# Kernel optimization log

Hardware: AMD Instinct MI355X
Metric: run time of the kernel (lower is better)

## Reference

```python
import jax, jax.numpy as jnp
import numpy as np

B, LQ, LK, DK, DV = 32, 128, 4096, 256, 256


def setup_inputs() -> dict:
    key = jax.random.key(0)
    k1, k2, k3, k4, k5 = jax.random.split(key, 5)
    return {
        "query": jax.random.normal(k1, (B, LQ, DK), dtype=jnp.float32),
        "query_lengths": jax.random.randint(k2, (B,), 1, LQ, dtype=jnp.int32),
        "keys": jax.random.normal(k3, (B, LK, DK), dtype=jnp.float32),
        "values": jax.random.normal(k4, (B, LK, DV), dtype=jnp.float32),
        "mask": jax.random.randint(k5, (B, LK), 0, 2, dtype=jnp.int32),  # 1 = masked out
    }


def reference(query, query_lengths, keys, values, mask):
    # zero query positions beyond each example's length (torch: mask_query masked_fill 0)
    q_valid = jnp.arange(query.shape[1])[None, :] < query_lengths[:, None]  # [B, Lq]
    query = jnp.where(q_valid[:, :, None], query, 0.0)
    # zero masked key/value timesteps (torch mask: 1 -> masked)
    kv_valid = (mask == 0)[:, :, None]  # [B, Lk, 1]
    keys = jnp.where(kv_valid, keys, 0.0)
    values = jnp.where(kv_valid, values, 0.0)
    # attention scores [B, Lq, Lk]
    weights = jnp.einsum("bqd,bkd->bqk", query, keys)
    # exact-zero scores (masked rows/cols) -> -inf, matching torch weights==0.0 fill
    weights = jnp.where(weights == 0.0, -jnp.inf, weights)
    weights = jax.nn.softmax(weights, axis=-1)
    # rows that were all -inf produce NaN -> cleaned to 0
    weights = jnp.where(jnp.isnan(weights), 0.0, weights)
    attended = jnp.einsum("bqk,bkv->bqv", weights, values)  # [B, Lq, Dv]
    return jnp.mean(attended, axis=1)  # [B, Dv]
```

## Files before the change

kernel.cpp:

```cpp
#include <hip/hip_runtime.h>
#include <hip/hip_fp16.h>
#include <stdint.h>

#define NB  32
#define NLQ 128
#define NLK 4096
#define NDK 256
#define NDV 256
#define KT  32
#define SPLITS 8
#define MINSPLITS 4

typedef _Float16 f16;
typedef _Float16 f16x4 __attribute__((ext_vector_type(4)));
typedef _Float16 f16x8 __attribute__((ext_vector_type(8)));
typedef float    f32x4 __attribute__((ext_vector_type(4)));

__global__ __launch_bounds__(512) void fvta_part1(
    const float* __restrict__ q_, const float* __restrict__ k_,
    const float* __restrict__ v_, const int* __restrict__ mask_,
    f16* __restrict__ accw, float* __restrict__ mlw)
{
    __shared__ __align__(16) f16 KA[2][KT * NDK];
    __shared__ __align__(16) f16 VA[2][KT * NDV];
    __shared__ int MK[NLK / MINSPLITS];

    const int tid = threadIdx.x, w = tid >> 6, lane = tid & 63;
    const int l15 = lane & 15, lhi = lane >> 4;
    const int qsub = w >> 1;
    const int dvh  = w & 1;
    const int x = blockIdx.x, b = blockIdx.y;
    const int S = gridDim.x >> 1;
    const int s = x >> 1, qz = x & 1;
    const int slice = NLK / S, nt = slice / KT, kbase = s * slice;
    const float NEG = -__builtin_inff();

    const float* kb = k_ + ((size_t)b * NLK + kbase) * NDK;
    const float* vb = v_ + ((size_t)b * NLK + kbase) * NDV;
    const int*   mb = mask_ + b * NLK + kbase;

    for (int i = tid; i < slice; i += 512) MK[i] = mb[i];

    f16x8 qf[8];
    {
        const float* qrow = q_ + ((size_t)b * NLQ + qz * 64 + qsub * 16 + l15) * NDK
                          + lhi * 8;
        #pragma unroll
        for (int kd = 0; kd < 8; ++kd) {
            f32x4 xv = *(const f32x4*)(qrow + kd * 32);
            f32x4 yv = *(const f32x4*)(qrow + kd * 32 + 4);
            f16x8 f;
            f[0]=(f16)xv[0]; f[1]=(f16)xv[1]; f[2]=(f16)xv[2]; f[3]=(f16)xv[3];
            f[4]=(f16)yv[0]; f[5]=(f16)yv[1]; f[6]=(f16)yv[2]; f[7]=(f16)yv[3];
            qf[kd] = f;
        }
    }

    f32x4 accu[8];
    #pragma unroll
    for (int i = 0; i < 8; ++i) accu[i] = (f32x4){0.f, 0.f, 0.f, 0.f};
    float m_run = NEG, l_run = 0.f;

    f32x4 ks[4], vs[4];

    auto stage = [&](f16* KAb, f16* VAb) {
        #pragma unroll
        for (int r = 0; r < 4; ++r) {
            const int idx = r * 512 + tid;
            const int kk  = idx >> 6;
            const int d   = (idx & 63) * 4;
            const int e   = kk * NDK + (d ^ ((kk & 15) << 3));
            f32x4 xv = ks[r];
            f16x4 hh; hh[0]=(f16)xv[0]; hh[1]=(f16)xv[1]; hh[2]=(f16)xv[2]; hh[3]=(f16)xv[3];
            *(f16x4*)(KAb + e) = hh;
            f32x4 yv = vs[r];
            f16x4 gg; gg[0]=(f16)yv[0]; gg[1]=(f16)yv[1]; gg[2]=(f16)yv[2]; gg[3]=(f16)yv[3];
            *(f16x4*)(VAb + e) = gg;
        }
    };

    #pragma unroll
    for (int r = 0; r < 4; ++r) {
        ks[r] = *(const f32x4*)(kb + (r * 512 + tid) * 4);
        vs[r] = *(const f32x4*)(vb + (r * 512 + tid) * 4);
    }
    stage(KA[0], VA[0]);
    __syncthreads();

    const int swz = l15 << 3;

    for (int t = 0; t < nt; ++t) {
        const int cur = t & 1;
        if (t + 1 < nt) {
            const float* ksrc = kb + (size_t)(t + 1) * KT * NDK;
            const float* vsrc = vb + (size_t)(t + 1) * KT * NDV;
            #pragma unroll
            for (int r = 0; r < 4; ++r) {
                ks[r] = *(const f32x4*)(ksrc + (r * 512 + tid) * 4);
                vs[r] = *(const f32x4*)(vsrc + (r * 512 + tid) * 4);
            }
        }
        const int k0 = t * KT;

        f32x4 s4a = (f32x4){0.f,0.f,0.f,0.f}, s4b = s4a;
        {
            const f16* k0p = &KA[cur][(0 * 16 + l15) * NDK];
            const f16* k1p = &KA[cur][(1 * 16 + l15) * NDK];
            #pragma unroll
            for (int kd = 0; kd < 8; ++kd) {
                const int col = (kd * 32 + lhi * 8) ^ swz;
                f16x8 kfa = *(const f16x8*)(k0p + col);
                s4a = __builtin_amdgcn_mfma_f32_16x16x32_f16(kfa, qf[kd], s4a, 0, 0, 0);
                f16x8 kfb = *(const f16x8*)(k1p + col);
                s4b = __builtin_amdgcn_mfma_f32_16x16x32_f16(kfb, qf[kd], s4b, 0, 0, 0);
            }
        }

        const int4 m4a = *(const int4*)(MK + k0 + lhi * 4);
        const int4 m4b = *(const int4*)(MK + k0 + 16 + lhi * 4);
        float sa[4], sb[4];
        sa[0] = m4a.x ? NEG : s4a[0]; sa[1] = m4a.y ? NEG : s4a[1];
        sa[2] = m4a.z ? NEG : s4a[2]; sa[3] = m4a.w ? NEG : s4a[3];
        sb[0] = m4b.x ? NEG : s4b[0]; sb[1] = m4b.y ? NEG : s4b[1];
        sb[2] = m4b.z ? NEG : s4b[2]; sb[3] = m4b.w ? NEG : s4b[3];

        float tmax = fmaxf(fmaxf(fmaxf(sa[0], sa[1]), fmaxf(sa[2], sa[3])),
                           fmaxf(fmaxf(sb[0], sb[1]), fmaxf(sb[2], sb[3])));
        tmax = fmaxf(tmax, __shfl_xor(tmax, 16, 64));
        tmax = fmaxf(tmax, __shfl_xor(tmax, 32, 64));

        const bool defer = (m_run != NEG) && __all(tmax - m_run <= 8.f);
        if (!defer) {
            const float mnew = fmaxf(m_run, tmax);
            if (mnew != NEG) {
                const float scale = (m_run == NEG) ? 0.f : __expf(m_run - mnew);
                float scj[4];
                #pragma unroll
                for (int j = 0; j < 4; ++j) scj[j] = __shfl(scale, lhi * 4 + j, 64);
                #pragma unroll
                for (int d = 0; d < 8; ++d) {
                    accu[d][0] *= scj[0]; accu[d][1] *= scj[1];
                    accu[d][2] *= scj[2]; accu[d][3] *= scj[3];
                }
                l_run *= scale;
                m_run = mnew;
            }
        }

        float p4a[4], p4b[4];
        if (m_run == NEG) {
            #pragma unroll
            for (int j = 0; j < 4; ++j) { p4a[j] = 0.f; p4b[j] = 0.f; }
        } else {
            #pragma unroll
            for (int j = 0; j < 4; ++j) {
                p4a[j] = __expf(sa[j] - m_run);
                p4b[j] = __expf(sb[j] - m_run);
            }
        }
        float ps = (p4a[0] + p4a[1]) + (p4a[2] + p4a[3])
                 + (p4b[0] + p4b[1]) + (p4b[2] + p4b[3]);
        ps += __shfl_xor(ps, 16, 64);
        ps += __shfl_xor(ps, 32, 64);
        l_run += ps;

        f16x4 pa, pb;
        pa[0]=(f16)p4a[0]; pa[1]=(f16)p4a[1]; pa[2]=(f16)p4a[2]; pa[3]=(f16)p4a[3];
        pb[0]=(f16)p4b[0]; pb[1]=(f16)p4b[1]; pb[2]=(f16)p4b[2]; pb[3]=(f16)p4b[3];

        {
            const f16* VL = &VA[cur][0];
            #pragma unroll
            for (int h = 0; h < 2; ++h) {
                const f16x4 pfrag = h ? pb : pa;
                #pragma unroll
                for (int dg = 0; dg < 2; ++dg) {
                    #pragma unroll
                    for (int dd = 0; dd < 4; ++dd) {
                        f16x4 vf;
                        #pragma unroll
                        for (int j = 0; j < 4; ++j) {
                            const int rr  = lhi * 4 + j;
                            const int row = h * 16 + rr;
                            const int col = (dvh * 128 + (dg * 4 + dd) * 16 + l15)
                                            ^ (rr << 3);
                            vf[j] = VL[row * NDV + col];
                        }
                        accu[dg * 4 + dd] = __builtin_amdgcn_mfma_f32_16x16x16f16(
                            pfrag, vf, accu[dg * 4 + dd], 0, 0, 0);
                    }
                }
            }
        }

        if (t + 1 < nt) stage(KA[cur ^ 1], VA[cur ^ 1]);
        __syncthreads();
    }

    const float rl = (l_run > 0.f) ? 1.f / l_run : 0.f;
    float rlj[4];
    #pragma unroll
    for (int j = 0; j < 4; ++j) rlj[j] = __shfl(rl, lhi * 4 + j, 64);

    const size_t base = (size_t)(b * S + s) * NLQ + qz * 64 + qsub * 16;
    #pragma unroll
    for (int j = 0; j < 4; ++j) {
        f16* dst = accw + (base + lhi * 4 + j) * NDV + dvh * 128 + l15;
        #pragma unroll
        for (int d = 0; d < 8; ++d) dst[d * 16] = (f16)(accu[d][j] * rlj[j]);
    }
    if (dvh == 0 && lane < 16) {
        mlw[(base + lane) * 2]     = m_run;
        mlw[(base + lane) * 2 + 1] = l_run;
    }
}

__global__ __launch_bounds__(256) void fvta_merge(
    const f16* __restrict__ accw, const float* __restrict__ mlw,
    const int* __restrict__ qlen_, float* __restrict__ out_, int S)
{
    __shared__ float fac[8][SPLITS + 1];
    const int qc = blockIdx.x, b = blockIdx.y, tid = threadIdx.x;
    const int len = qlen_[b];
    const float NEG = -__builtin_inff();

    if (tid < 8) {
        const int q = qc * 8 + tid;
        if (q < len) {
            float gm = NEG;
            for (int ss = 0; ss < S; ++ss)
                gm = fmaxf(gm, mlw[((size_t)(b * S + ss) * NLQ + q) * 2]);
            float L = 0.f;
            for (int ss = 0; ss < S; ++ss) {
                const float m = mlw[((size_t)(b * S + ss) * NLQ + q) * 2];
                const float l = mlw[((size_t)(b * S + ss) * NLQ + q) * 2 + 1];
                if (m != NEG) L += l * __expf(m - gm);
            }
            for (int ss = 0; ss < S; ++ss) {
                const float m = mlw[((size_t)(b * S + ss) * NLQ + q) * 2];
                const float l = mlw[((size_t)(b * S + ss) * NLQ + q) * 2 + 1];
                fac[tid][ss] = (gm != NEG && L > 0.f && m != NEG)
                             ? l * __expf(m - gm) / L : 0.f;
            }
        } else {
            for (int ss = 0; ss < S; ++ss) fac[tid][ss] = 0.f;
        }
    }
    __syncthreads();

    float sum = 0.f;
    for (int qq = 0; qq < 8; ++qq) {
        const int q = qc * 8 + qq;
        for (int ss = 0; ss < S; ++ss) {
            const float f = fac[qq][ss];
            if (f != 0.f)
                sum += (float)accw[((size_t)(b * S + ss) * NLQ + q) * NDV + tid] * f;
        }
    }
    atomicAdd(&out_[b * NDV + tid], sum * (1.f / NLQ));
}

extern "C" void kernel_launch(void* const* d_in, const int* in_sizes, int n_in,
                              void* d_out, int out_size, void* d_ws, size_t ws_size,
                              hipStream_t stream) {
    const float* q    = (const float*)d_in[0];
    const int*   qlen = (const int*)d_in[1];
    const float* k    = (const float*)d_in[2];
    const float* v    = (const float*)d_in[3];
    const int*   mask = (const int*)d_in[4];
    float* out = (float*)d_out;

    int S = SPLITS;
    while (S > MINSPLITS &&
           ((size_t)NB * S * NLQ * NDV * 2 + (size_t)NB * S * NLQ * 8) > ws_size)
        S >>= 1;
    f16*   accw = (f16*)d_ws;
    float* mlw  = (float*)((char*)d_ws + (size_t)NB * S * NLQ * NDV * 2);

    hipMemsetAsync(out, 0, (size_t)out_size * sizeof(float), stream);
    dim3 g1(2 * S, NB);
    fvta_part1<<<g1, 512, 0, stream>>>(q, k, v, mask, accw, mlw);
    dim3 g2(NLQ / 8, NB);
    fvta_merge<<<g2, 256, 0, stream>>>(accw, mlw, qlen, out, S);
}
```

Measured before the change: 127.8 us.

## Store V transposed in LDS and use 16x16x32 MFMA for PV

V tiles are now loaded column-wise from global memory, each thread reading 16 strided floats, and written to LDS in a transposed, k-grouped layout. The PV product can then read contiguous f16x8 fragments and issue 8 MFMA 16x16x32 ops instead of 16 MFMA 16x16x16 ops fed by scalar LDS gathers. The P fragment is rebuilt with lane shuffles to match the new operand layout. The cost is uncoalesced strided global loads of V and extra shuffle work per tile.

```diff
diff --git a/kernel.cpp b/kernel.cpp
--- a/kernel.cpp
+++ b/kernel.cpp
@@ -12,6 +12,7 @@
 #define MINSPLITS 4
 
 typedef _Float16 f16;
+typedef _Float16 f16x2 __attribute__((ext_vector_type(2)));
 typedef _Float16 f16x4 __attribute__((ext_vector_type(4)));
 typedef _Float16 f16x8 __attribute__((ext_vector_type(8)));
 typedef float    f32x4 __attribute__((ext_vector_type(4)));
@@ -22,7 +23,7 @@
     f16* __restrict__ accw, float* __restrict__ mlw)
 {
     __shared__ __align__(16) f16 KA[2][KT * NDK];
-    __shared__ __align__(16) f16 VA[2][KT * NDV];
+    __shared__ __align__(16) f16 VT[2][4 * NDV * 8];
     __shared__ int MK[NLK / MINSPLITS];
 
     const int tid = threadIdx.x, w = tid >> 6, lane = tid & 63;
@@ -61,9 +62,11 @@
     for (int i = 0; i < 8; ++i) accu[i] = (f32x4){0.f, 0.f, 0.f, 0.f};
     float m_run = NEG, l_run = 0.f;
 
-    f32x4 ks[4], vs[4];
-
-    auto stage = [&](f16* KAb, f16* VAb) {
+    f32x4 ks[4];
+    float vsv[16];
+    const int dvv = tid >> 1, gv = tid & 1;
+
+    auto stageK = [&](f16* KAb) {
         #pragma unroll
         for (int r = 0; r < 4; ++r) {
             const int idx = r * 512 + tid;
@@ -73,33 +76,35 @@
             f32x4 xv = ks[r];
             f16x4 hh; hh[0]=(f16)xv[0]; hh[1]=(f16)xv[1]; hh[2]=(f16)xv[2]; hh[3]=(f16)xv[3];
             *(f16x4*)(KAb + e) = hh;
-            f32x4 yv = vs[r];
-            f16x4 gg; gg[0]=(f16)yv[0]; gg[1]=(f16)yv[1]; gg[2]=(f16)yv[2]; gg[3]=(f16)yv[3];
-            *(f16x4*)(VAb + e) = gg;
         }
     };
-
-    #pragma unroll
-    for (int r = 0; r < 4; ++r) {
-        ks[r] = *(const f32x4*)(kb + (r * 512 + tid) * 4);
-        vs[r] = *(const f32x4*)(vb + (r * 512 + tid) * 4);
-    }
-    stage(KA[0], VA[0]);
+    auto stageV = [&](f16* VTb) {
+        f16x8 lo, hi;
+        #pragma unroll
+        for (int i = 0; i < 8; ++i) { lo[i] = (f16)vsv[i]; hi[i] = (f16)vsv[8 + i]; }
+        *(f16x8*)(VTb + (2 * gv)     * (NDV * 8) + dvv * 8) = lo;
+        *(f16x8*)(VTb + (2 * gv + 1) * (NDV * 8) + dvv * 8) = hi;
+    };
+    auto loadKV = [&](int t) {
+        const float* ksrc = kb + (size_t)t * KT * NDK;
+        #pragma unroll
+        for (int r = 0; r < 4; ++r)
+            ks[r] = *(const f32x4*)(ksrc + (r * 512 + tid) * 4);
+        const float* vsrc = vb + (size_t)t * KT * NDV + gv * 16 * NDV + dvv;
+        #pragma unroll
+        for (int i = 0; i < 16; ++i)
+            vsv[i] = vsrc[i * NDV];
+    };
+
+    loadKV(0);
+    stageK(KA[0]); stageV(VT[0]);
     __syncthreads();
 
     const int swz = l15 << 3;
 
     for (int t = 0; t < nt; ++t) {
         const int cur = t & 1;
-        if (t + 1 < nt) {
-            const float* ksrc = kb + (size_t)(t + 1) * KT * NDK;
-            const float* vsrc = vb + (size_t)(t + 1) * KT * NDV;
-            #pragma unroll
-            for (int r = 0; r < 4; ++r) {
-                ks[r] = *(const f32x4*)(ksrc + (r * 512 + tid) * 4);
-                vs[r] = *(const f32x4*)(vsrc + (r * 512 + tid) * 4);
-            }
-        }
+        if (t + 1 < nt) loadKV(t + 1);
         const int k0 = t * KT;
 
         f32x4 s4a = (f32x4){0.f,0.f,0.f,0.f}, s4b = s4a;
@@ -164,36 +169,38 @@
         ps += __shfl_xor(ps, 32, 64);
         l_run += ps;
 
-        f16x4 pa, pb;
-        pa[0]=(f16)p4a[0]; pa[1]=(f16)p4a[1]; pa[2]=(f16)p4a[2]; pa[3]=(f16)p4a[3];
-        pb[0]=(f16)p4b[0]; pb[1]=(f16)p4b[1]; pb[2]=(f16)p4b[2]; pb[3]=(f16)p4b[3];
-
+        f16x8 pfrag;
         {
-            const f16* VL = &VA[cur][0];
-            #pragma unroll
-            for (int h = 0; h < 2; ++h) {
-                const f16x4 pfrag = h ? pb : pa;
-                #pragma unroll
-                for (int dg = 0; dg < 2; ++dg) {
-                    #pragma unroll
-                    for (int dd = 0; dd < 4; ++dd) {
-                        f16x4 vf;
-                        #pragma unroll
-                        for (int j = 0; j < 4; ++j) {
-                            const int rr  = lhi * 4 + j;
-                            const int row = h * 16 + rr;
-                            const int col = (dvh * 128 + (dg * 4 + dd) * 16 + l15)
-                                            ^ (rr << 3);
-                            vf[j] = VL[row * NDV + col];
-                        }
-                        accu[dg * 4 + dd] = __builtin_amdgcn_mfma_f32_16x16x16f16(
-                            pfrag, vf, accu[dg * 4 + dd], 0, 0, 0);
-                    }
-                }
-            }
-        }
-
-        if (t + 1 < nt) stage(KA[cur ^ 1], VA[cur ^ 1]);
+            union PU { f16x2 h; int u; } A0, A1, B0, B1;
+            A0.h[0]=(f16)p4a[0]; A0.h[1]=(f16)p4a[1];
+            A1.h[0]=(f16)p4a[2]; A1.h[1]=(f16)p4a[3];
+            B0.h[0]=(f16)p4b[0]; B0.h[1]=(f16)p4b[1];
+            B1.h[0]=(f16)p4b[2]; B1.h[1]=(f16)p4b[3];
+            const int sf = l15 + ((lhi & 1) << 5);
+            const int ss = sf + 16;
+            const int a0 = __shfl(A0.u, sf, 64), a1 = __shfl(A1.u, sf, 64);
+            const int b0 = __shfl(B0.u, sf, 64), b1 = __shfl(B1.u, sf, 64);
+            const int a2 = __shfl(A0.u, ss, 64), a3 = __shfl(A1.u, ss, 64);
+            const int b2 = __shfl(B0.u, ss, 64), b3 = __shfl(B1.u, ss, 64);
+            const bool useB = (lhi >= 2);
+            union PW { int u[4]; f16x8 v; } pw;
+            pw.u[0] = useB ? b0 : a0; pw.u[1] = useB ? b1 : a1;
+            pw.u[2] = useB ? b2 : a2; pw.u[3] = useB ? b3 : a3;
+            pfrag = pw.v;
+        }
+
+        {
+            const f16* vbase = &VT[cur][0] + lhi * (NDV * 8)
+                             + (dvh * 128 + l15) * 8;
+            #pragma unroll
+            for (int dc = 0; dc < 8; ++dc) {
+                f16x8 vf = *(const f16x8*)(vbase + dc * 16 * 8);
+                accu[dc] = __builtin_amdgcn_mfma_f32_16x16x32_f16(
+                    pfrag, vf, accu[dc], 0, 0, 0);
+            }
+        }
+
+        if (t + 1 < nt) { stageK(KA[cur ^ 1]); stageV(VT[cur ^ 1]); }
         __syncthreads();
     }
 
```

Result: slower. 138.3 us (+8.2%).

## Stage only half of V in LDS; read other half directly from global

Applied to the files above, without the earlier changes.

Only the first 128 value columns are staged into LDS as fp16. Waves handling the upper half load their V fragments straight from global memory inside the PV loop and convert them in registers. This halves the V shared-memory footprint and staging stores, which may improve occupancy. In exchange, the global loads sit on the critical path with uncoalesced strided access and no prefetch, so latency may be exposed.

```diff
diff --git a/kernel.cpp b/kernel.cpp
--- a/kernel.cpp
+++ b/kernel.cpp
@@ -22,7 +22,7 @@
     f16* __restrict__ accw, float* __restrict__ mlw)
 {
     __shared__ __align__(16) f16 KA[2][KT * NDK];
-    __shared__ __align__(16) f16 VA[2][KT * NDV];
+    __shared__ __align__(16) f16 VA[2][KT * 128];
     __shared__ int MK[NLK / MINSPLITS];
 
     const int tid = threadIdx.x, w = tid >> 6, lane = tid & 63;
@@ -61,7 +61,7 @@
     for (int i = 0; i < 8; ++i) accu[i] = (f32x4){0.f, 0.f, 0.f, 0.f};
     float m_run = NEG, l_run = 0.f;
 
-    f32x4 ks[4], vs[4];
+    f32x4 ks[4], vs[2];
 
     auto stage = [&](f16* KAb, f16* VAb) {
         #pragma unroll
@@ -73,17 +73,34 @@
             f32x4 xv = ks[r];
             f16x4 hh; hh[0]=(f16)xv[0]; hh[1]=(f16)xv[1]; hh[2]=(f16)xv[2]; hh[3]=(f16)xv[3];
             *(f16x4*)(KAb + e) = hh;
+        }
+        #pragma unroll
+        for (int r = 0; r < 2; ++r) {
+            const int idx = r * 512 + tid;
+            const int kk  = idx >> 5;
+            const int d   = (idx & 31) * 4;
+            const int e   = kk * 128 + (d ^ ((kk & 15) << 3));
             f32x4 yv = vs[r];
             f16x4 gg; gg[0]=(f16)yv[0]; gg[1]=(f16)yv[1]; gg[2]=(f16)yv[2]; gg[3]=(f16)yv[3];
             *(f16x4*)(VAb + e) = gg;
         }
     };
-
-    #pragma unroll
-    for (int r = 0; r < 4; ++r) {
-        ks[r] = *(const f32x4*)(kb + (r * 512 + tid) * 4);
-        vs[r] = *(const f32x4*)(vb + (r * 512 + tid) * 4);
-    }
+    auto loadKV = [&](int t) {
+        const float* ksrc = kb + (size_t)t * KT * NDK;
+        #pragma unroll
+        for (int r = 0; r < 4; ++r)
+            ks[r] = *(const f32x4*)(ksrc + (r * 512 + tid) * 4);
+        const float* vsrc = vb + (size_t)t * KT * NDV;
+        #pragma unroll
+        for (int r = 0; r < 2; ++r) {
+            const int idx = r * 512 + tid;
+            const int kk  = idx >> 5;
+            const int d   = (idx & 31) * 4;
+            vs[r] = *(const f32x4*)(vsrc + kk * NDV + d);
+        }
+    };
+
+    loadKV(0);
     stage(KA[0], VA[0]);
     __syncthreads();
 
@@ -91,15 +108,7 @@
 
     for (int t = 0; t < nt; ++t) {
         const int cur = t & 1;
-        if (t + 1 < nt) {
-            const float* ksrc = kb + (size_t)(t + 1) * KT * NDK;
-            const float* vsrc = vb + (size_t)(t + 1) * KT * NDV;
-            #pragma unroll
-            for (int r = 0; r < 4; ++r) {
-                ks[r] = *(const f32x4*)(ksrc + (r * 512 + tid) * 4);
-                vs[r] = *(const f32x4*)(vsrc + (r * 512 + tid) * 4);
-            }
-        }
+        if (t + 1 < nt) loadKV(t + 1);
         const int k0 = t * KT;
 
         f32x4 s4a = (f32x4){0.f,0.f,0.f,0.f}, s4b = s4a;
@@ -168,7 +177,7 @@
         pa[0]=(f16)p4a[0]; pa[1]=(f16)p4a[1]; pa[2]=(f16)p4a[2]; pa[3]=(f16)p4a[3];
         pb[0]=(f16)p4b[0]; pb[1]=(f16)p4b[1]; pb[2]=(f16)p4b[2]; pb[3]=(f16)p4b[3];
 
-        {
+        if (dvh == 0) {
             const f16* VL = &VA[cur][0];
             #pragma unroll
             for (int h = 0; h < 2; ++h) {
@@ -182,10 +191,36 @@
                         for (int j = 0; j < 4; ++j) {
                             const int rr  = lhi * 4 + j;
                             const int row = h * 16 + rr;
-                            const int col = (dvh * 128 + (dg * 4 + dd) * 16 + l15)
-                                            ^ (rr << 3);
-                            vf[j] = VL[row * NDV + col];
+                            const int col = ((dg * 4 + dd) * 16 + l15) ^ (rr << 3);
+                            vf[j] = VL[row * 128 + col];
                         }
+                        accu[dg * 4 + dd] = __builtin_amdgcn_mfma_f32_16x16x16f16(
+                            pfrag, vf, accu[dg * 4 + dd], 0, 0, 0);
+                    }
+                }
+            }
+        } else {
+            #pragma unroll
+            for (int h = 0; h < 2; ++h) {
+                const f16x4 pfrag = h ? pb : pa;
+                const float* vr = vb + (size_t)(k0 + h * 16 + lhi * 4) * NDV
+                                + 128 + l15;
+                #pragma unroll
+                for (int dg = 0; dg < 2; ++dg) {
+                    float tv[4][4];
+                    #pragma unroll
+                    for (int dd = 0; dd < 4; ++dd) {
+                        const float* vc = vr + (dg * 4 + dd) * 16;
+                        tv[dd][0] = vc[0];
+                        tv[dd][1] = vc[1 * NDV];
+                        tv[dd][2] = vc[2 * NDV];
+                        tv[dd][3] = vc[3 * NDV];
+                    }
+                    #pragma unroll
+                    for (int dd = 0; dd < 4; ++dd) {
+                        f16x4 vf;
+                        vf[0]=(f16)tv[dd][0]; vf[1]=(f16)tv[dd][1];
+                        vf[2]=(f16)tv[dd][2]; vf[3]=(f16)tv[dd][3];
                         accu[dg * 4 + dd] = __builtin_amdgcn_mfma_f32_16x16x16f16(
                             pfrag, vf, accu[dg * 4 + dd], 0, 0, 0);
                     }
```

New measurement: 137.6 us. +7.6%, slower.
